# Performance work log

Measured on AMD Instinct MI355X. Metric: run time of the kernel, lower is better.

The kernel has to match this reference:

```python
import jax, jax.numpy as jnp
import numpy as np

EPS = 1e-5  # BatchNorm eps


def _conv_bn_tanh(h, w, b, g, be, m, v):
    # 3x3 conv, stride 1, SAME padding (pad = k//2), NCHW / OIHW
    y = jax.lax.conv_general_dilated(
        h, w, window_strides=(1, 1), padding='SAME',
        dimension_numbers=('NCHW', 'OIHW', 'NCHW'))
    y = y + b[None, :, None, None]
    # BatchNorm inference: gamma * (y - mean) / sqrt(var + eps) + beta
    scale = g * jax.lax.rsqrt(v + EPS)
    y = y * scale[None, :, None, None] + (be - m * scale)[None, :, None, None]
    return jnp.tanh(y)


def _unfold3x3(x):
    # torch F.unfold(k=3, pad=1, stride=1) -> (N, C, 9, H, W), kernel positions row-major
    N, C, H, W = x.shape
    xp = jnp.pad(x, ((0, 0), (0, 0), (1, 1), (1, 1)))
    patches = [xp[:, :, i:i + H, j:j + W] for i in range(3) for j in range(3)]
    return jnp.stack(patches, axis=2)  # (N, C, 9, H, W)


def setup_inputs() -> dict:
    key = jax.random.key(0)
    ks = jax.random.split(key, 24)
    N, C, H, W = 8, 64, 128, 128
    INTER, FEAT, NB, KK = 64, 6, 6, 9
    d = {}
    d['x'] = jax.random.normal(ks[0], (N, C, H, W), jnp.float32)
    d['w0'] = jax.random.normal(ks[1], (INTER, C, 3, 3), jnp.float32) * 0.05
    d['b0'] = jax.random.normal(ks[2], (INTER,), jnp.float32) * 0.05
    d['g0'] = jax.random.uniform(ks[3], (INTER,), jnp.float32)
    d['be0'] = jax.random.normal(ks[4], (INTER,), jnp.float32) * 0.05
    d['m0'] = jax.random.normal(ks[5], (INTER,), jnp.float32) * 0.05
    d['v0'] = jax.random.uniform(ks[6], (INTER,), jnp.float32)
    d['wm'] = jax.random.normal(ks[7], (5, INTER, INTER, 3, 3), jnp.float32) * 0.05
    d['bm'] = jax.random.normal(ks[8], (5, INTER), jnp.float32) * 0.05
    d['gm'] = jax.random.uniform(ks[9], (5, INTER), jnp.float32)
    d['bem'] = jax.random.normal(ks[10], (5, INTER), jnp.float32) * 0.05
    d['mm'] = jax.random.normal(ks[11], (5, INTER), jnp.float32) * 0.05
    d['vm'] = jax.random.uniform(ks[12], (5, INTER), jnp.float32)
    OC = FEAT * NB  # 36
    d['wl'] = jax.random.normal(ks[13], (OC, INTER, 3, 3), jnp.float32) * 0.05
    d['bl'] = jax.random.normal(ks[14], (OC,), jnp.float32) * 0.05
    d['gl'] = jax.random.uniform(ks[15], (OC,), jnp.float32)
    d['bel'] = jax.random.normal(ks[16], (OC,), jnp.float32) * 0.05
    d['ml'] = jax.random.normal(ks[17], (OC,), jnp.float32) * 0.05
    d['vl'] = jax.random.uniform(ks[18], (OC,), jnp.float32)
    d['bases'] = jax.random.normal(ks[19], (NB, KK), jnp.float32)  # FB bases buffer (6, 9)
    return d


def reference(x, w0, b0, g0, be0, m0, v0, wm, bm, gm, bem, mm, vm,
              wl, bl, gl, bel, ml, vl, bases):
    N, C, H, W = x.shape
    FEAT, NB = 6, 6
    # bases_net: conv-bn-tanh x7 (eval mode, dropout no-ops)
    h = _conv_bn_tanh(x, w0, b0, g0, be0, m0, v0)
    for i in range(5):
        h = _conv_bn_tanh(h, wm[i], bm[i], gm[i], bem[i], mm[i], vm[i])
    h = _conv_bn_tanh(h, wl, bl, gl, bel, ml, vl)  # (N, 36, H, W)
    bfeat = h.reshape(N, FEAT, NB, H, W)
    # per-pixel basis coefficients: (N, M, 9, H, W)
    bcoef = jnp.einsum('bmkhw,kl->bmlhw', bfeat, bases)
    patches = _unfold3x3(x)  # (N, C, 9, H, W)
    # dynamic conv: combine per-pixel coeffs with unfolded input
    out = jnp.einsum('bmlhw,bclhw->bcmhw', bcoef, patches)  # (N, C, M, H, W)
    return out.reshape(N, C * NB, H, W)
```

## Files before the change

kernel.cpp:

```cpp
#include <hip/hip_runtime.h>
#include <hip/hip_bf16.h>

typedef short bf16x4 __attribute__((ext_vector_type(4)));
typedef short bf16x8 __attribute__((ext_vector_type(8)));
typedef float f32x4  __attribute__((ext_vector_type(4)));

__device__ inline unsigned short f2us(float f) {
    __hip_bfloat16 h = __float2bfloat16(f);
    return *(unsigned short*)&h;
}
__device__ inline float us2f(unsigned short u) {
    union { unsigned int i; float f; } c; c.i = ((unsigned int)u) << 16; return c.f;
}
__device__ inline float tanh_fast(float x) {
    float xs = fminf(fmaxf(x, -20.f), 20.f);
    float t = __expf(2.f * xs);
    return 1.f - 2.f / (t + 1.f);
}

__device__ inline void gload_lds16(const void* g, void* l) {
    __builtin_amdgcn_global_load_lds(
        (const __attribute__((address_space(1))) void*)g,
        (__attribute__((address_space(3))) void*)l,
        16, 0, 0);
}

__global__ __launch_bounds__(256)
void prep_all(const float* __restrict__ x, unsigned short* __restrict__ xcl,
              const float* __restrict__ w0, const float* __restrict__ wm,
              const float* __restrict__ wl, unsigned short* __restrict__ Wf,
              const float* b0, const float* g0, const float* be0,
              const float* m0, const float* v0,
              const float* bm, const float* gm, const float* bem,
              const float* mm, const float* vm,
              const float* bl, const float* gl, const float* bel,
              const float* ml, const float* vl,
              float* __restrict__ Af, float* __restrict__ Bf,
              unsigned int* __restrict__ zp)
{
    const int bid = blockIdx.x;
    const int t = threadIdx.x;
    if (bid < 1024) {
        __shared__ unsigned short t2[128 * 68];
        int n = bid >> 7, h = bid & 127;
        const float* xp = x + (size_t)n * 64 * 16384 + h * 128;
        for (int i = t; i < 8192; i += 256) {
            int ci = i >> 7, w = i & 127;
            t2[w * 68 + ci] = f2us(xp[(size_t)ci * 16384 + w]);
        }
        __syncthreads();
        unsigned short* op = xcl + ((size_t)(n * 16384 + h * 128)) * 64;
        for (int i = t; i < 1024; i += 256) {
            int w = i >> 3, c8 = i & 7;
            union { bf16x4 v[2]; uint4 q; } u;
            u.v[0] = *(bf16x4*)&t2[w * 68 + c8 * 8];
            u.v[1] = *(bf16x4*)&t2[w * 68 + c8 * 8 + 4];
            *(uint4*)(op + w * 64 + c8 * 8) = u.q;
        }
    } else if (bid < 2032) {
        int idx = (bid - 1024) * 256 + t;
        int l = idx / 36864, r = idx - l * 36864;
        int tp = r >> 12, r2 = r & 4095;
        int hh = r2 >> 11, nb = (r2 >> 9) & 3, ln = (r2 >> 3) & 63, j = r2 & 7;
        int ci = hh * 32 + (ln >> 4) * 8 + j;
        int co = (ln & 15) * 4 + nb;
        float val = 0.f;
        if (l < 6) {
            const float* src = (l == 0) ? w0 : (wm + (size_t)(l - 1) * 36864);
            val = src[(co * 64 + ci) * 9 + tp];
        } else if (co < 36) {
            val = wl[(co * 64 + ci) * 9 + tp];
        }
        Wf[idx] = f2us(val);
    } else {
        int idx = (bid - 2032) * 256 + t;
        if (bid == 2033 && t >= 192) zp[t - 192] = 0u;
        if (idx < 448) {
            int l = idx >> 6, c = idx & 63;
            float b, g, be, m, v;
            bool zero = false;
            if (l == 0) {
                b = b0[c]; g = g0[c]; be = be0[c]; m = m0[c]; v = v0[c];
            } else if (l < 6) {
                int o = (l - 1) * 64 + c;
                b = bm[o]; g = gm[o]; be = bem[o]; m = mm[o]; v = vm[o];
            } else if (c < 36) {
                b = bl[c]; g = gl[c]; be = bel[c]; m = ml[c]; v = vl[c];
            } else zero = true;
            if (zero) { Af[idx] = 0.f; Bf[idx] = 0.f; }
            else {
                float s = g / sqrtf(v + 1e-5f);
                Af[idx] = s;
                Bf[idx] = (b - m) * s + be;
            }
        }
    }
}

#define LDS_W_OFF 78336
__global__ __launch_bounds__(512, 2)
void conv_mfma(const unsigned short* __restrict__ src,
               const unsigned short* __restrict__ Wf,
               const float* __restrict__ A, const float* __restrict__ B,
               unsigned short* __restrict__ dst,
               const unsigned short* __restrict__ zp)
{
    __shared__ __align__(16) unsigned char smem[152064];
    const int n = blockIdx.z;
    const int h0 = blockIdx.y * 16, w0 = blockIdx.x * 32;
    const int t = threadIdx.x;
    const int ln = t & 63, wv = t >> 6;
    const int xln = ln & 15, qd = ln >> 4;
    const size_t ibase = (size_t)n * 16384 * 64;

    const unsigned short* srcn = src + ibase;
    for (int i = wv; i < 77; i += 8) {
        int g = i * 64 + ln;
        int p = g >> 3, jj = g & 7;
        int ty = (p * 1928) >> 16;
        int tx = p - ty * 34;
        int gy = h0 + ty - 1, gx = w0 + tx - 1;
        int js = jj ^ (p & 7);
        const unsigned short* gsrc =
            (((unsigned)gy < 128u) & ((unsigned)gx < 128u))
                ? srcn + (ptrdiff_t)(gy * 128 + gx) * 64 + js * 8
                : zp;
        if (g < 4896) gload_lds16(gsrc, smem + (size_t)i * 1024);
    }
    for (int i = wv; i < 72; i += 8) {
        const unsigned short* gsrc = Wf + ((size_t)(i * 64 + ln)) * 8;
        gload_lds16(gsrc, smem + LDS_W_OFF + (size_t)i * 1024);
    }
    __syncthreads();

    f32x4 acc[2][2][4];
#pragma unroll
    for (int rh = 0; rh < 2; ++rh)
#pragma unroll
        for (int hf = 0; hf < 2; ++hf)
#pragma unroll
            for (int nb = 0; nb < 4; ++nb)
                acc[rh][hf][nb] = (f32x4){0.f, 0.f, 0.f, 0.f};

    const int rbase = wv * 2;
#pragma unroll
    for (int tp = 0; tp < 9; ++tp) {
        const int ky = tp / 3, kx = tp % 3;
        bf16x8 b[2][4];
#pragma unroll
        for (int hh = 0; hh < 2; ++hh)
#pragma unroll
            for (int nb = 0; nb < 4; ++nb)
                b[hh][nb] = *(const bf16x8*)(smem + LDS_W_OFF +
                    (((((tp * 2 + hh) * 4 + nb) * 64) + ln) << 4));
#pragma unroll
        for (int rh = 0; rh < 2; ++rh) {
#pragma unroll
            for (int hf = 0; hf < 2; ++hf) {
                const int p = (rbase + rh + ky) * 34 + hf * 16 + xln + kx;
                const int pb = p * 128, sw = (p & 7) << 4;
#pragma unroll
                for (int hh = 0; hh < 2; ++hh) {
                    bf16x8 a = *(const bf16x8*)(smem + pb +
                                                (((qd + 4 * hh) << 4) ^ sw));
#pragma unroll
                    for (int nb = 0; nb < 4; ++nb)
                        acc[rh][hf][nb] = __builtin_amdgcn_mfma_f32_16x16x32_bf16(
                            a, b[hh][nb], acc[rh][hf][nb], 0, 0, 0);
                }
            }
        }
    }

    const float4 A4 = *(const float4*)&A[xln * 4];
    const float4 B4 = *(const float4*)&B[xln * 4];
#pragma unroll
    for (int rh = 0; rh < 2; ++rh) {
        const int gy = h0 + rbase + rh;
        unsigned short* dp = dst + ibase + (size_t)(gy * 128) * 64 + xln * 4;
#pragma unroll
        for (int hf = 0; hf < 2; ++hf) {
#pragma unroll
            for (int r = 0; r < 4; ++r) {
                const int gx = w0 + hf * 16 + qd * 4 + r;
                ushort4 o;
                o.x = f2us(tanh_fast(fmaf(acc[rh][hf][0][r], A4.x, B4.x)));
                o.y = f2us(tanh_fast(fmaf(acc[rh][hf][1][r], A4.y, B4.y)));
                o.z = f2us(tanh_fast(fmaf(acc[rh][hf][2][r], A4.z, B4.z)));
                o.w = f2us(tanh_fast(fmaf(acc[rh][hf][3][r], A4.w, B4.w)));
                *(ushort4*)(dp + (size_t)gx * 64) = o;
            }
        }
    }
}

__global__ __launch_bounds__(256)
void dyn_conv(const float* __restrict__ x, const unsigned short* __restrict__ h7,
              const float* __restrict__ bases, float* __restrict__ out)
{
    __shared__ float tile[32 * 10 * 34];
    const int n = blockIdx.z;
    const int h0 = blockIdx.y * 8, w0 = blockIdx.x * 32;
    const float* xp = x + (size_t)n * 64 * 16384;
    const int t = threadIdx.x;
    const int tw = t & 31, th = t >> 5;
    const int h = h0 + th, w = w0 + tw;

    float bs[54];
#pragma unroll
    for (int i = 0; i < 54; ++i) bs[i] = bases[i];

    union { uint4 q[5]; unsigned short s[40]; } hv;
    const unsigned short* hp = h7 + (size_t)(n * 16384 + h * 128 + w) * 64;
#pragma unroll
    for (int i = 0; i < 5; ++i) hv.q[i] = ((const uint4*)hp)[i];

    float coef[54];
#pragma unroll
    for (int i = 0; i < 54; ++i) coef[i] = 0.f;
#pragma unroll
    for (int m = 0; m < 6; ++m)
#pragma unroll
        for (int k = 0; k < 6; ++k) {
            float f = us2f(hv.s[m * 6 + k]);
#pragma unroll
            for (int l = 0; l < 9; ++l)
                coef[m * 9 + l] = fmaf(f, bs[k * 9 + l], coef[m * 9 + l]);
        }

    float* op = out + (size_t)n * 384 * 16384 + h * 128 + w;

    for (int half = 0; half < 2; ++half) {
        if (half) __syncthreads();
        for (int idx = t; idx < 32 * 340; idx += 256) {
            int ci = idx / 340, r = idx % 340, y = r / 34, xw = r % 34;
            int gy = h0 + y - 1, gx = w0 + xw - 1;
            float v = 0.f;
            if ((unsigned)gy < 128u && (unsigned)gx < 128u)
                v = xp[(size_t)(half * 32 + ci) * 16384 + gy * 128 + gx];
            tile[idx] = v;
        }
        __syncthreads();

#pragma unroll 1
        for (int c = 0; c < 32; ++c) {
            float xv[9];
#pragma unroll
            for (int ky = 0; ky < 3; ++ky)
#pragma unroll
                for (int kx = 0; kx < 3; ++kx)
                    xv[ky * 3 + kx] = tile[c * 340 + (th + ky) * 34 + (tw + kx)];
            int cg = half * 32 + c;
#pragma unroll
            for (int m = 0; m < 6; ++m) {
                float s = 0.f;
#pragma unroll
                for (int l = 0; l < 9; ++l) s = fmaf(coef[m * 9 + l], xv[l], s);
                op[(size_t)(cg * 6 + m) * 16384] = s;
            }
        }
    }
}

extern "C" void kernel_launch(void* const* d_in, const int* in_sizes, int n_in,
                              void* d_out, int out_size, void* d_ws, size_t ws_size,
                              hipStream_t stream)
{
    const float* x   = (const float*)d_in[0];
    const float* w0  = (const float*)d_in[1];
    const float* b0  = (const float*)d_in[2];
    const float* g0  = (const float*)d_in[3];
    const float* be0 = (const float*)d_in[4];
    const float* m0  = (const float*)d_in[5];
    const float* v0  = (const float*)d_in[6];
    const float* wm  = (const float*)d_in[7];
    const float* bm  = (const float*)d_in[8];
    const float* gm  = (const float*)d_in[9];
    const float* bem = (const float*)d_in[10];
    const float* mm  = (const float*)d_in[11];
    const float* vm  = (const float*)d_in[12];
    const float* wl  = (const float*)d_in[13];
    const float* bl  = (const float*)d_in[14];
    const float* gl  = (const float*)d_in[15];
    const float* bel = (const float*)d_in[16];
    const float* ml  = (const float*)d_in[17];
    const float* vl  = (const float*)d_in[18];
    const float* bas = (const float*)d_in[19];

    unsigned short* Wfb = (unsigned short*)d_ws;
    float* Af  = (float*)((char*)d_ws + 524288);
    float* Bf  = Af + 448;
    unsigned int* zp = (unsigned int*)((char*)d_ws + (1 << 20));
    unsigned short* xcl  = (unsigned short*)((char*)d_ws + (size_t)(2  << 20));
    unsigned short* bufA = (unsigned short*)((char*)d_ws + (size_t)(2  << 20) + 16777216);
    unsigned short* bufB = (unsigned short*)((char*)d_ws + (size_t)(2  << 20) + 2 * 16777216);

    prep_all<<<2034, 256, 0, stream>>>(x, xcl, w0, wm, wl, Wfb,
                                       b0, g0, be0, m0, v0,
                                       bm, gm, bem, mm, vm,
                                       bl, gl, bel, ml, vl, Af, Bf, zp);

    dim3 cg(4, 8, 8);
    const unsigned short* zps = (const unsigned short*)zp;
    conv_mfma<<<cg, 512, 0, stream>>>(xcl,  Wfb + 0 * 36864, Af + 0,   Bf + 0,   bufA, zps);
    conv_mfma<<<cg, 512, 0, stream>>>(bufA, Wfb + 1 * 36864, Af + 64,  Bf + 64,  bufB, zps);
    conv_mfma<<<cg, 512, 0, stream>>>(bufB, Wfb + 2 * 36864, Af + 128, Bf + 128, bufA, zps);
    conv_mfma<<<cg, 512, 0, stream>>>(bufA, Wfb + 3 * 36864, Af + 192, Bf + 192, bufB, zps);
    conv_mfma<<<cg, 512, 0, stream>>>(bufB, Wfb + 4 * 36864, Af + 256, Bf + 256, bufA, zps);
    conv_mfma<<<cg, 512, 0, stream>>>(bufA, Wfb + 5 * 36864, Af + 320, Bf + 320, bufB, zps);
    conv_mfma<<<cg, 512, 0, stream>>>(bufB, Wfb + 6 * 36864, Af + 384, Bf + 384, bufA, zps);

    dim3 dg(4, 16, 8);
    dyn_conv<<<dg, 256, 0, stream>>>(x, bufA, bas, (float*)d_out);
}
```

Baseline: 403.7 us.

## Fuse all stages into one cooperative persistent kernel with grid syncs

Replaces the prep kernel, the seven conv launches and the dynamic-conv kernel with a single cooperative kernel of 256 persistent blocks that use grid.sync between stages. Each block keeps its tile resident in LDS across layers, reloads only its interior tile before the barrier and the halo after it, and prefetches the next layer's weights into registers during the epilogue. This is meant to remove launch gaps and redundant LDS reloads. In exchange it adds grid-wide barrier cost, limits the grid to 256 blocks so occupancy is fixed, and reworks the dyn_conv tiling to 512 threads.

```diff
diff --git a/kernel.cpp b/kernel.cpp
--- a/kernel.cpp
+++ b/kernel.cpp
@@ -1,5 +1,8 @@
 #include <hip/hip_runtime.h>
 #include <hip/hip_bf16.h>
+#include <hip/hip_cooperative_groups.h>
+
+namespace cg = cooperative_groups;
 
 typedef short bf16x4 __attribute__((ext_vector_type(4)));
 typedef short bf16x8 __attribute__((ext_vector_type(8)));
@@ -25,238 +28,298 @@
         16, 0, 0);
 }
 
-__global__ __launch_bounds__(256)
-void prep_all(const float* __restrict__ x, unsigned short* __restrict__ xcl,
-              const float* __restrict__ w0, const float* __restrict__ wm,
-              const float* __restrict__ wl, unsigned short* __restrict__ Wf,
-              const float* b0, const float* g0, const float* be0,
-              const float* m0, const float* v0,
-              const float* bm, const float* gm, const float* bem,
-              const float* mm, const float* vm,
-              const float* bl, const float* gl, const float* bel,
-              const float* ml, const float* vl,
-              float* __restrict__ Af, float* __restrict__ Bf,
-              unsigned int* __restrict__ zp)
+struct MegaArgs {
+    const float *x, *w0, *b0, *g0, *be0, *m0, *v0;
+    const float *wm, *bm, *gm, *bem, *mm, *vm;
+    const float *wl, *bl, *gl, *bel, *ml, *vl, *bas;
+    unsigned short *Wfb, *xcl, *bufA, *bufB;
+    float *Af, *Bf, *out;
+    unsigned int *zp;
+};
+
+#define LDS_W_OFF 78336
+
+__global__ __launch_bounds__(512, 2) void mega(MegaArgs g)
 {
+    __shared__ __align__(16) unsigned char smem[152064];
     const int bid = blockIdx.x;
     const int t = threadIdx.x;
-    if (bid < 1024) {
-        __shared__ unsigned short t2[128 * 68];
-        int n = bid >> 7, h = bid & 127;
-        const float* xp = x + (size_t)n * 64 * 16384 + h * 128;
-        for (int i = t; i < 8192; i += 256) {
-            int ci = i >> 7, w = i & 127;
-            t2[w * 68 + ci] = f2us(xp[(size_t)ci * 16384 + w]);
-        }
-        __syncthreads();
-        unsigned short* op = xcl + ((size_t)(n * 16384 + h * 128)) * 64;
-        for (int i = t; i < 1024; i += 256) {
-            int w = i >> 3, c8 = i & 7;
-            union { bf16x4 v[2]; uint4 q; } u;
-            u.v[0] = *(bf16x4*)&t2[w * 68 + c8 * 8];
-            u.v[1] = *(bf16x4*)&t2[w * 68 + c8 * 8 + 4];
-            *(uint4*)(op + w * 64 + c8 * 8) = u.q;
-        }
-    } else if (bid < 2032) {
-        int idx = (bid - 1024) * 256 + t;
-        int l = idx / 36864, r = idx - l * 36864;
-        int tp = r >> 12, r2 = r & 4095;
-        int hh = r2 >> 11, nb = (r2 >> 9) & 3, ln = (r2 >> 3) & 63, j = r2 & 7;
-        int ci = hh * 32 + (ln >> 4) * 8 + j;
-        int co = (ln & 15) * 4 + nb;
-        float val = 0.f;
-        if (l < 6) {
-            const float* src = (l == 0) ? w0 : (wm + (size_t)(l - 1) * 36864);
-            val = src[(co * 64 + ci) * 9 + tp];
-        } else if (co < 36) {
-            val = wl[(co * 64 + ci) * 9 + tp];
-        }
-        Wf[idx] = f2us(val);
-    } else {
-        int idx = (bid - 2032) * 256 + t;
-        if (bid == 2033 && t >= 192) zp[t - 192] = 0u;
-        if (idx < 448) {
-            int l = idx >> 6, c = idx & 63;
-            float b, g, be, m, v;
+    const int ln = t & 63, wv = t >> 6;
+    cg::grid_group grid = cg::this_grid();
+
+    {
+        unsigned short* t2 = (unsigned short*)smem;
+        for (int k = 0; k < 4; ++k) {
+            int tid = bid * 4 + k;
+            int pn = tid >> 7, ph = tid & 127;
+            const float* xp = g.x + (size_t)pn * 64 * 16384 + ph * 128;
+            if (k) __syncthreads();
+            for (int i = t; i < 8192; i += 512) {
+                int ci = i >> 7, w = i & 127;
+                t2[w * 68 + ci] = f2us(xp[(size_t)ci * 16384 + w]);
+            }
+            __syncthreads();
+            unsigned short* op = g.xcl + ((size_t)(pn * 16384 + ph * 128)) * 64;
+            for (int i = t; i < 1024; i += 512) {
+                int w = i >> 3, c8 = i & 7;
+                union { bf16x4 v[2]; uint4 q; } u;
+                u.v[0] = *(bf16x4*)&t2[w * 68 + c8 * 8];
+                u.v[1] = *(bf16x4*)&t2[w * 68 + c8 * 8 + 4];
+                *(uint4*)(op + w * 64 + c8 * 8) = u.q;
+            }
+        }
+        for (int j = t; j < 1008; j += 512) {
+            int idx = bid * 1008 + j;
+            int l = idx / 36864, r = idx - l * 36864;
+            int tp = r >> 12, r2 = r & 4095;
+            int hh = r2 >> 11, nb = (r2 >> 9) & 3, lw = (r2 >> 3) & 63, jc = r2 & 7;
+            int ci = hh * 32 + (lw >> 4) * 8 + jc;
+            int co = (lw & 15) * 4 + nb;
+            float val = 0.f;
+            if (l < 6) {
+                const float* s0 = (l == 0) ? g.w0 : (g.wm + (size_t)(l - 1) * 36864);
+                val = s0[(co * 64 + ci) * 9 + tp];
+            } else if (co < 36) {
+                val = g.wl[(co * 64 + ci) * 9 + tp];
+            }
+            g.Wfb[idx] = f2us(val);
+        }
+        if (bid == 0 && t < 448) {
+            int l = t >> 6, c = t & 63;
+            float b, ga, be, m, v;
             bool zero = false;
             if (l == 0) {
-                b = b0[c]; g = g0[c]; be = be0[c]; m = m0[c]; v = v0[c];
+                b = g.b0[c]; ga = g.g0[c]; be = g.be0[c]; m = g.m0[c]; v = g.v0[c];
             } else if (l < 6) {
                 int o = (l - 1) * 64 + c;
-                b = bm[o]; g = gm[o]; be = bem[o]; m = mm[o]; v = vm[o];
+                b = g.bm[o]; ga = g.gm[o]; be = g.bem[o]; m = g.mm[o]; v = g.vm[o];
             } else if (c < 36) {
-                b = bl[c]; g = gl[c]; be = bel[c]; m = ml[c]; v = vl[c];
+                b = g.bl[c]; ga = g.gl[c]; be = g.bel[c]; m = g.ml[c]; v = g.vl[c];
             } else zero = true;
-            if (zero) { Af[idx] = 0.f; Bf[idx] = 0.f; }
+            if (zero) { g.Af[t] = 0.f; g.Bf[t] = 0.f; }
             else {
-                float s = g / sqrtf(v + 1e-5f);
-                Af[idx] = s;
-                Bf[idx] = (b - m) * s + be;
-            }
-        }
+                float s = ga / sqrtf(v + 1e-5f);
+                g.Af[t] = s;
+                g.Bf[t] = (b - m) * s + be;
+            }
+        }
+        if (bid == 1 && t < 64) g.zp[t] = 0u;
     }
-}
-
-#define LDS_W_OFF 78336
-__global__ __launch_bounds__(512, 2)
-void conv_mfma(const unsigned short* __restrict__ src,
-               const unsigned short* __restrict__ Wf,
-               const float* __restrict__ A, const float* __restrict__ B,
-               unsigned short* __restrict__ dst,
-               const unsigned short* __restrict__ zp)
-{
-    __shared__ __align__(16) unsigned char smem[152064];
-    const int n = blockIdx.z;
-    const int h0 = blockIdx.y * 16, w0 = blockIdx.x * 32;
-    const int t = threadIdx.x;
-    const int ln = t & 63, wv = t >> 6;
+    grid.sync();
+
+    const int bx = bid & 3, by = (bid >> 2) & 7, cn = bid >> 5;
+    const int h0 = by * 16, w0c = bx * 32;
+    const size_t ibase = (size_t)cn * 16384 * 64;
     const int xln = ln & 15, qd = ln >> 4;
-    const size_t ibase = (size_t)n * 16384 * 64;
-
-    const unsigned short* srcn = src + ibase;
-    for (int i = wv; i < 77; i += 8) {
-        int g = i * 64 + ln;
-        int p = g >> 3, jj = g & 7;
-        int ty = (p * 1928) >> 16;
-        int tx = p - ty * 34;
-        int gy = h0 + ty - 1, gx = w0 + tx - 1;
-        int js = jj ^ (p & 7);
-        const unsigned short* gsrc =
-            (((unsigned)gy < 128u) & ((unsigned)gx < 128u))
-                ? srcn + (ptrdiff_t)(gy * 128 + gx) * 64 + js * 8
-                : zp;
-        if (g < 4896) gload_lds16(gsrc, smem + (size_t)i * 1024);
+    const int rbase = wv * 2;
+    uint4 wpre[9];
+
+    {
+        const unsigned short* srcn = g.xcl + ibase;
+        for (int i = wv; i < 77; i += 8) {
+            int gg = i * 64 + ln;
+            int p = gg >> 3, jj = gg & 7;
+            int ty = (p * 1928) >> 16;
+            int tx = p - ty * 34;
+            int gy = h0 + ty - 1, gx = w0c + tx - 1;
+            int js = jj ^ (p & 7);
+            const unsigned short* gsrc =
+                (((unsigned)gy < 128u) & ((unsigned)gx < 128u))
+                    ? srcn + (ptrdiff_t)(gy * 128 + gx) * 64 + js * 8
+                    : (const unsigned short*)g.zp;
+            if (gg < 4896) gload_lds16(gsrc, smem + (size_t)i * 1024);
+        }
+        for (int i = wv; i < 72; i += 8)
+            gload_lds16(g.Wfb + ((size_t)(i * 64 + ln)) * 8,
+                        smem + LDS_W_OFF + (size_t)i * 1024);
+        __syncthreads();
     }
-    for (int i = wv; i < 72; i += 8) {
-        const unsigned short* gsrc = Wf + ((size_t)(i * 64 + ln)) * 8;
-        gload_lds16(gsrc, smem + LDS_W_OFF + (size_t)i * 1024);
+
+#pragma unroll 1
+    for (int l = 0; l < 7; ++l) {
+        unsigned short* dstp = (l & 1) ? g.bufB : g.bufA;
+
+        f32x4 acc[2][2][4];
+#pragma unroll
+        for (int rh = 0; rh < 2; ++rh)
+#pragma unroll
+            for (int hf = 0; hf < 2; ++hf)
+#pragma unroll
+                for (int nb = 0; nb < 4; ++nb)
+                    acc[rh][hf][nb] = (f32x4){0.f, 0.f, 0.f, 0.f};
+
+#pragma unroll
+        for (int tp = 0; tp < 9; ++tp) {
+            const int ky = tp / 3, kx = tp % 3;
+            bf16x8 b[2][4];
+#pragma unroll
+            for (int hh = 0; hh < 2; ++hh)
+#pragma unroll
+                for (int nb = 0; nb < 4; ++nb)
+                    b[hh][nb] = *(const bf16x8*)(smem + LDS_W_OFF +
+                        (((((tp * 2 + hh) * 4 + nb) * 64) + ln) << 4));
+#pragma unroll
+            for (int rh = 0; rh < 2; ++rh) {
+#pragma unroll
+                for (int hf = 0; hf < 2; ++hf) {
+                    const int p = (rbase + rh + ky) * 34 + hf * 16 + xln + kx;
+                    const int pb = p * 128, sw = (p & 7) << 4;
+#pragma unroll
+                    for (int hh = 0; hh < 2; ++hh) {
+                        bf16x8 a = *(const bf16x8*)(smem + pb +
+                                                    (((qd + 4 * hh) << 4) ^ sw));
+#pragma unroll
+                        for (int nb = 0; nb < 4; ++nb)
+                            acc[rh][hf][nb] = __builtin_amdgcn_mfma_f32_16x16x32_bf16(
+                                a, b[hh][nb], acc[rh][hf][nb], 0, 0, 0);
+                    }
+                }
+            }
+        }
+
+        if (l < 6) {
+            const uint4* wnext = (const uint4*)(g.Wfb + (size_t)(l + 1) * 36864);
+#pragma unroll
+            for (int k = 0; k < 9; ++k) wpre[k] = wnext[t + 512 * k];
+        }
+
+        {
+            const float* Ap = g.Af + l * 64;
+            const float* Bp = g.Bf + l * 64;
+            const float4 A4 = *(const float4*)&Ap[xln * 4];
+            const float4 B4 = *(const float4*)&Bp[xln * 4];
+#pragma unroll
+            for (int rh = 0; rh < 2; ++rh) {
+                const int gy = h0 + rbase + rh;
+                unsigned short* dp = dstp + ibase + (size_t)(gy * 128) * 64 + xln * 4;
+#pragma unroll
+                for (int hf = 0; hf < 2; ++hf) {
+#pragma unroll
+                    for (int r = 0; r < 4; ++r) {
+                        const int gx = w0c + hf * 16 + qd * 4 + r;
+                        ushort4 o;
+                        o.x = f2us(tanh_fast(fmaf(acc[rh][hf][0][r], A4.x, B4.x)));
+                        o.y = f2us(tanh_fast(fmaf(acc[rh][hf][1][r], A4.y, B4.y)));
+                        o.z = f2us(tanh_fast(fmaf(acc[rh][hf][2][r], A4.z, B4.z)));
+                        o.w = f2us(tanh_fast(fmaf(acc[rh][hf][3][r], A4.w, B4.w)));
+                        *(ushort4*)(dp + (size_t)gx * 64) = o;
+                    }
+                }
+            }
+        }
+        if (l == 6) break;
+
+        __threadfence();
+        __syncthreads();
+
+        const unsigned short* srcn = dstp + ibase;
+        for (int i = wv; i < 64; i += 8) {
+            int p = i * 8 + (ln >> 3), jj = ln & 7;
+            int ty = 1 + (p >> 5), tx = 1 + (p & 31);
+            int pp = ty * 34 + tx;
+            int gy = h0 + ty - 1, gx = w0c + tx - 1;
+            int js = jj ^ (pp & 7);
+            gload_lds16(srcn + (ptrdiff_t)(gy * 128 + gx) * 64 + js * 8,
+                        smem + (size_t)((1 + (i >> 2)) * 34 + 1 + (i & 3) * 8) * 128);
+        }
+
+        grid.sync();
+
+        for (int i = wv; i < 10; i += 8) {
+            int row = (i < 5) ? 0 : 17;
+            int i5 = (i < 5) ? i : i - 5;
+            int pir = i5 * 8 + (ln >> 3), jj = ln & 7;
+            int pp = row * 34 + pir;
+            int gy = h0 + row - 1, gx = w0c + pir - 1;
+            int js = jj ^ (pp & 7);
+            const unsigned short* gsrc =
+                (((unsigned)gy < 128u) & ((unsigned)gx < 128u))
+                    ? srcn + (ptrdiff_t)(gy * 128 + gx) * 64 + js * 8
+                    : (const unsigned short*)g.zp;
+            if (pir < 34) gload_lds16(gsrc, smem + (size_t)(row * 34 + i5 * 8) * 128);
+        }
+        if (t < 256) {
+            int k2 = t >> 3, jj = t & 7;
+            int ty = 1 + (k2 >> 1), tx = (k2 & 1) * 33;
+            int pp = ty * 34 + tx;
+            int gy = h0 + ty - 1, gx = w0c + tx - 1;
+            uint4 v = make_uint4(0u, 0u, 0u, 0u);
+            if ((unsigned)gx < 128u)
+                v = *(const uint4*)(srcn + (ptrdiff_t)(gy * 128 + gx) * 64 + jj * 8);
+            *(uint4*)(smem + (size_t)pp * 128 + ((size_t)(jj ^ (pp & 7)) << 4)) = v;
+        }
+        {
+            uint4* wdst = (uint4*)(smem + LDS_W_OFF);
+#pragma unroll
+            for (int k = 0; k < 9; ++k) wdst[t + 512 * k] = wpre[k];
+        }
+        __syncthreads();
     }
-    __syncthreads();
-
-    f32x4 acc[2][2][4];
-#pragma unroll
-    for (int rh = 0; rh < 2; ++rh)
-#pragma unroll
-        for (int hf = 0; hf < 2; ++hf)
-#pragma unroll
-            for (int nb = 0; nb < 4; ++nb)
-                acc[rh][hf][nb] = (f32x4){0.f, 0.f, 0.f, 0.f};
-
-    const int rbase = wv * 2;
-#pragma unroll
-    for (int tp = 0; tp < 9; ++tp) {
-        const int ky = tp / 3, kx = tp % 3;
-        bf16x8 b[2][4];
-#pragma unroll
-        for (int hh = 0; hh < 2; ++hh)
-#pragma unroll
-            for (int nb = 0; nb < 4; ++nb)
-                b[hh][nb] = *(const bf16x8*)(smem + LDS_W_OFF +
-                    (((((tp * 2 + hh) * 4 + nb) * 64) + ln) << 4));
-#pragma unroll
-        for (int rh = 0; rh < 2; ++rh) {
-#pragma unroll
-            for (int hf = 0; hf < 2; ++hf) {
-                const int p = (rbase + rh + ky) * 34 + hf * 16 + xln + kx;
-                const int pb = p * 128, sw = (p & 7) << 4;
-#pragma unroll
-                for (int hh = 0; hh < 2; ++hh) {
-                    bf16x8 a = *(const bf16x8*)(smem + pb +
-                                                (((qd + 4 * hh) << 4) ^ sw));
-#pragma unroll
-                    for (int nb = 0; nb < 4; ++nb)
-                        acc[rh][hf][nb] = __builtin_amdgcn_mfma_f32_16x16x32_bf16(
-                            a, b[hh][nb], acc[rh][hf][nb], 0, 0, 0);
+
+    grid.sync();
+
+    {
+        float* tile = (float*)smem;
+        const int dn = bid >> 5, ti = bid & 31;
+        const int h0d = (ti >> 1) * 8, w0d = (ti & 1) * 64;
+        const float* xp = g.x + (size_t)dn * 64 * 16384;
+        const int tw = t & 63, th = t >> 6;
+        const int h = h0d + th, w = w0d + tw;
+
+        float bs[54];
+#pragma unroll
+        for (int i = 0; i < 54; ++i) bs[i] = g.bas[i];
+
+        union { uint4 q[5]; unsigned short s[40]; } hv;
+        const unsigned short* hp = g.bufA + (size_t)(dn * 16384 + h * 128 + w) * 64;
+#pragma unroll
+        for (int i = 0; i < 5; ++i) hv.q[i] = ((const uint4*)hp)[i];
+
+        float coef[54];
+#pragma unroll
+        for (int i = 0; i < 54; ++i) coef[i] = 0.f;
+#pragma unroll
+        for (int m = 0; m < 6; ++m)
+#pragma unroll
+            for (int k = 0; k < 6; ++k) {
+                float f = us2f(hv.s[m * 6 + k]);
+#pragma unroll
+                for (int lq = 0; lq < 9; ++lq)
+                    coef[m * 9 + lq] = fmaf(f, bs[k * 9 + lq], coef[m * 9 + lq]);
+            }
+
+        float* op = g.out + (size_t)dn * 384 * 16384 + h * 128 + w;
+
+        for (int half = 0; half < 2; ++half) {
+            if (half) __syncthreads();
+            for (int idx = t; idx < 21120; idx += 512) {
+                int ci = idx / 660, r = idx - ci * 660;
+                int y = r / 66, xw = r - y * 66;
+                int gy = h0d + y - 1, gx = w0d + xw - 1;
+                float v = 0.f;
+                if ((unsigned)gy < 128u && (unsigned)gx < 128u)
+                    v = xp[(size_t)(half * 32 + ci) * 16384 + gy * 128 + gx];
+                tile[idx] = v;
+            }
+            __syncthreads();
+
+#pragma unroll 1
+            for (int c = 0; c < 32; ++c) {
+                float xv[9];
+#pragma unroll
+                for (int ky = 0; ky < 3; ++ky)
+#pragma unroll
+                    for (int kx = 0; kx < 3; ++kx)
+                        xv[ky * 3 + kx] = tile[c * 660 + (th + ky) * 66 + (tw + kx)];
+                int cgc = half * 32 + c;
+#pragma unroll
+                for (int m = 0; m < 6; ++m) {
+                    float s = 0.f;
+#pragma unroll
+                    for (int lq = 0; lq < 9; ++lq)
+                        s = fmaf(coef[m * 9 + lq], xv[lq], s);
+                    op[(size_t)(cgc * 6 + m) * 16384] = s;
                 }
-            }
-        }
-    }
-
-    const float4 A4 = *(const float4*)&A[xln * 4];
-    const float4 B4 = *(const float4*)&B[xln * 4];
-#pragma unroll
-    for (int rh = 0; rh < 2; ++rh) {
-        const int gy = h0 + rbase + rh;
-        unsigned short* dp = dst + ibase + (size_t)(gy * 128) * 64 + xln * 4;
-#pragma unroll
-        for (int hf = 0; hf < 2; ++hf) {
-#pragma unroll
-            for (int r = 0; r < 4; ++r) {
-                const int gx = w0 + hf * 16 + qd * 4 + r;
-                ushort4 o;
-                o.x = f2us(tanh_fast(fmaf(acc[rh][hf][0][r], A4.x, B4.x)));
-                o.y = f2us(tanh_fast(fmaf(acc[rh][hf][1][r], A4.y, B4.y)));
-                o.z = f2us(tanh_fast(fmaf(acc[rh][hf][2][r], A4.z, B4.z)));
-                o.w = f2us(tanh_fast(fmaf(acc[rh][hf][3][r], A4.w, B4.w)));
-                *(ushort4*)(dp + (size_t)gx * 64) = o;
-            }
-        }
-    }
-}
-
-__global__ __launch_bounds__(256)
-void dyn_conv(const float* __restrict__ x, const unsigned short* __restrict__ h7,
-              const float* __restrict__ bases, float* __restrict__ out)
-{
-    __shared__ float tile[32 * 10 * 34];
-    const int n = blockIdx.z;
-    const int h0 = blockIdx.y * 8, w0 = blockIdx.x * 32;
-    const float* xp = x + (size_t)n * 64 * 16384;
-    const int t = threadIdx.x;
-    const int tw = t & 31, th = t >> 5;
-    const int h = h0 + th, w = w0 + tw;
-
-    float bs[54];
-#pragma unroll
-    for (int i = 0; i < 54; ++i) bs[i] = bases[i];
-
-    union { uint4 q[5]; unsigned short s[40]; } hv;
-    const unsigned short* hp = h7 + (size_t)(n * 16384 + h * 128 + w) * 64;
-#pragma unroll
-    for (int i = 0; i < 5; ++i) hv.q[i] = ((const uint4*)hp)[i];
-
-    float coef[54];
-#pragma unroll
-    for (int i = 0; i < 54; ++i) coef[i] = 0.f;
-#pragma unroll
-    for (int m = 0; m < 6; ++m)
-#pragma unroll
-        for (int k = 0; k < 6; ++k) {
-            float f = us2f(hv.s[m * 6 + k]);
-#pragma unroll
-            for (int l = 0; l < 9; ++l)
-                coef[m * 9 + l] = fmaf(f, bs[k * 9 + l], coef[m * 9 + l]);
-        }
-
-    float* op = out + (size_t)n * 384 * 16384 + h * 128 + w;
-
-    for (int half = 0; half < 2; ++half) {
-        if (half) __syncthreads();
-        for (int idx = t; idx < 32 * 340; idx += 256) {
-            int ci = idx / 340, r = idx % 340, y = r / 34, xw = r % 34;
-            int gy = h0 + y - 1, gx = w0 + xw - 1;
-            float v = 0.f;
-            if ((unsigned)gy < 128u && (unsigned)gx < 128u)
-                v = xp[(size_t)(half * 32 + ci) * 16384 + gy * 128 + gx];
-            tile[idx] = v;
-        }
-        __syncthreads();
-
-#pragma unroll 1
-        for (int c = 0; c < 32; ++c) {
-            float xv[9];
-#pragma unroll
-            for (int ky = 0; ky < 3; ++ky)
-#pragma unroll
-                for (int kx = 0; kx < 3; ++kx)
-                    xv[ky * 3 + kx] = tile[c * 340 + (th + ky) * 34 + (tw + kx)];
-            int cg = half * 32 + c;
-#pragma unroll
-            for (int m = 0; m < 6; ++m) {
-                float s = 0.f;
-#pragma unroll
-                for (int l = 0; l < 9; ++l) s = fmaf(coef[m * 9 + l], xv[l], s);
-                op[(size_t)(cg * 6 + m) * 16384] = s;
             }
         }
     }
@@ -266,50 +329,37 @@
                               void* d_out, int out_size, void* d_ws, size_t ws_size,
                               hipStream_t stream)
 {
-    const float* x   = (const float*)d_in[0];
-    const float* w0  = (const float*)d_in[1];
-    const float* b0  = (const float*)d_in[2];
-    const float* g0  = (const float*)d_in[3];
-    const float* be0 = (const float*)d_in[4];
-    const float* m0  = (const float*)d_in[5];
-    const float* v0  = (const float*)d_in[6];
-    const float* wm  = (const float*)d_in[7];
-    const float* bm  = (const float*)d_in[8];
-    const float* gm  = (const float*)d_in[9];
-    const float* bem = (const float*)d_in[10];
-    const float* mm  = (const float*)d_in[11];
-    const float* vm  = (const float*)d_in[12];
-    const float* wl  = (const float*)d_in[13];
-    const float* bl  = (const float*)d_in[14];
-    const float* gl  = (const float*)d_in[15];
-    const float* bel = (const float*)d_in[16];
-    const float* ml  = (const float*)d_in[17];
-    const float* vl  = (const float*)d_in[18];
-    const float* bas = (const float*)d_in[19];
-
-    unsigned short* Wfb = (unsigned short*)d_ws;
-    float* Af  = (float*)((char*)d_ws + 524288);
-    float* Bf  = Af + 448;
-    unsigned int* zp = (unsigned int*)((char*)d_ws + (1 << 20));
-    unsigned short* xcl  = (unsigned short*)((char*)d_ws + (size_t)(2  << 20));
-    unsigned short* bufA = (unsigned short*)((char*)d_ws + (size_t)(2  << 20) + 16777216);
-    unsigned short* bufB = (unsigned short*)((char*)d_ws + (size_t)(2  << 20) + 2 * 16777216);
-
-    prep_all<<<2034, 256, 0, stream>>>(x, xcl, w0, wm, wl, Wfb,
-                                       b0, g0, be0, m0, v0,
-                                       bm, gm, bem, mm, vm,
-                                       bl, gl, bel, ml, vl, Af, Bf, zp);
-
-    dim3 cg(4, 8, 8);
-    const unsigned short* zps = (const unsigned short*)zp;
-    conv_mfma<<<cg, 512, 0, stream>>>(xcl,  Wfb + 0 * 36864, Af + 0,   Bf + 0,   bufA, zps);
-    conv_mfma<<<cg, 512, 0, stream>>>(bufA, Wfb + 1 * 36864, Af + 64,  Bf + 64,  bufB, zps);
-    conv_mfma<<<cg, 512, 0, stream>>>(bufB, Wfb + 2 * 36864, Af + 128, Bf + 128, bufA, zps);
-    conv_mfma<<<cg, 512, 0, stream>>>(bufA, Wfb + 3 * 36864, Af + 192, Bf + 192, bufB, zps);
-    conv_mfma<<<cg, 512, 0, stream>>>(bufB, Wfb + 4 * 36864, Af + 256, Bf + 256, bufA, zps);
-    conv_mfma<<<cg, 512, 0, stream>>>(bufA, Wfb + 5 * 36864, Af + 320, Bf + 320, bufB, zps);
-    conv_mfma<<<cg, 512, 0, stream>>>(bufB, Wfb + 6 * 36864, Af + 384, Bf + 384, bufA, zps);
-
-    dim3 dg(4, 16, 8);
-    dyn_conv<<<dg, 256, 0, stream>>>(x, bufA, bas, (float*)d_out);
-}
+    MegaArgs a;
+    a.x   = (const float*)d_in[0];
+    a.w0  = (const float*)d_in[1];
+    a.b0  = (const float*)d_in[2];
+    a.g0  = (const float*)d_in[3];
+    a.be0 = (const float*)d_in[4];
+    a.m0  = (const float*)d_in[5];
+    a.v0  = (const float*)d_in[6];
+    a.wm  = (const float*)d_in[7];
+    a.bm  = (const float*)d_in[8];
+    a.gm  = (const float*)d_in[9];
+    a.bem = (const float*)d_in[10];
+    a.mm  = (const float*)d_in[11];
+    a.vm  = (const float*)d_in[12];
+    a.wl  = (const float*)d_in[13];
+    a.bl  = (const float*)d_in[14];
+    a.gl  = (const float*)d_in[15];
+    a.bel = (const float*)d_in[16];
+    a.ml  = (const float*)d_in[17];
+    a.vl  = (const float*)d_in[18];
+    a.bas = (const float*)d_in[19];
+
+    a.Wfb  = (unsigned short*)d_ws;
+    a.Af   = (float*)((char*)d_ws + 524288);
+    a.Bf   = a.Af + 448;
+    a.zp   = (unsigned int*)((char*)d_ws + (1 << 20));
+    a.xcl  = (unsigned short*)((char*)d_ws + (size_t)(2 << 20));
+    a.bufA = (unsigned short*)((char*)d_ws + (size_t)(2 << 20) + 16777216);
+    a.bufB = (unsigned short*)((char*)d_ws + (size_t)(2 << 20) + 2 * 16777216);
+    a.out  = (float*)d_out;
+
+    void* ka[] = {&a};
+    hipLaunchCooperativeKernel((const void*)mega, dim3(256), dim3(512), ka, 0, stream);
+}
```

Result: slower. 979.7 us (+142.7%).

## Fuse last conv layer with dynamic convolution, keeping features in LDS

Applied to the files above, without the earlier changes.

Merges the seventh conv-bn-tanh layer into the dynamic-conv kernel. The per-pixel basis features are written to shared memory in a swizzled layout instead of a global buffer, then read back for the coefficient and patch combination. This removes one kernel launch and a global write/read of the intermediate feature map. In exchange, the dynamic-conv stage now runs with the conv kernel's tile shape and 16-row blocks, reusing the same large LDS buffer, which may lower occupancy.

```diff
diff --git a/kernel.cpp b/kernel.cpp
--- a/kernel.cpp
+++ b/kernel.cpp
@@ -194,26 +194,122 @@
     }
 }
 
-__global__ __launch_bounds__(256)
-void dyn_conv(const float* __restrict__ x, const unsigned short* __restrict__ h7,
-              const float* __restrict__ bases, float* __restrict__ out)
+__global__ __launch_bounds__(512, 2)
+void conv6_dyn(const unsigned short* __restrict__ src,
+               const unsigned short* __restrict__ Wf,
+               const float* __restrict__ A, const float* __restrict__ B,
+               const float* __restrict__ x, const float* __restrict__ bases,
+               float* __restrict__ out,
+               const unsigned short* __restrict__ zp)
 {
-    __shared__ float tile[32 * 10 * 34];
+    __shared__ __align__(16) unsigned char smem[152064];
     const int n = blockIdx.z;
-    const int h0 = blockIdx.y * 8, w0 = blockIdx.x * 32;
-    const float* xp = x + (size_t)n * 64 * 16384;
+    const int h0 = blockIdx.y * 16, w0 = blockIdx.x * 32;
     const int t = threadIdx.x;
-    const int tw = t & 31, th = t >> 5;
-    const int h = h0 + th, w = w0 + tw;
+    const int ln = t & 63, wv = t >> 6;
+    const int xln = ln & 15, qd = ln >> 4;
+    const size_t ibase = (size_t)n * 16384 * 64;
+
+    const unsigned short* srcn = src + ibase;
+    for (int i = wv; i < 77; i += 8) {
+        int g = i * 64 + ln;
+        int p = g >> 3, jj = g & 7;
+        int ty = (p * 1928) >> 16;
+        int tx = p - ty * 34;
+        int gy = h0 + ty - 1, gx = w0 + tx - 1;
+        int js = jj ^ (p & 7);
+        const unsigned short* gsrc =
+            (((unsigned)gy < 128u) & ((unsigned)gx < 128u))
+                ? srcn + (ptrdiff_t)(gy * 128 + gx) * 64 + js * 8
+                : zp;
+        if (g < 4896) gload_lds16(gsrc, smem + (size_t)i * 1024);
+    }
+    for (int i = wv; i < 72; i += 8) {
+        const unsigned short* gsrc = Wf + ((size_t)(i * 64 + ln)) * 8;
+        gload_lds16(gsrc, smem + LDS_W_OFF + (size_t)i * 1024);
+    }
+    __syncthreads();
+
+    f32x4 acc[2][2][4];
+#pragma unroll
+    for (int rh = 0; rh < 2; ++rh)
+#pragma unroll
+        for (int hf = 0; hf < 2; ++hf)
+#pragma unroll
+            for (int nb = 0; nb < 4; ++nb)
+                acc[rh][hf][nb] = (f32x4){0.f, 0.f, 0.f, 0.f};
+
+    const int rbase = wv * 2;
+#pragma unroll
+    for (int tp = 0; tp < 9; ++tp) {
+        const int ky = tp / 3, kx = tp % 3;
+        bf16x8 b[2][4];
+#pragma unroll
+        for (int hh = 0; hh < 2; ++hh)
+#pragma unroll
+            for (int nb = 0; nb < 4; ++nb)
+                b[hh][nb] = *(const bf16x8*)(smem + LDS_W_OFF +
+                    (((((tp * 2 + hh) * 4 + nb) * 64) + ln) << 4));
+#pragma unroll
+        for (int rh = 0; rh < 2; ++rh) {
+#pragma unroll
+            for (int hf = 0; hf < 2; ++hf) {
+                const int p = (rbase + rh + ky) * 34 + hf * 16 + xln + kx;
+                const int pb = p * 128, sw = (p & 7) << 4;
+#pragma unroll
+                for (int hh = 0; hh < 2; ++hh) {
+                    bf16x8 a = *(const bf16x8*)(smem + pb +
+                                                (((qd + 4 * hh) << 4) ^ sw));
+#pragma unroll
+                    for (int nb = 0; nb < 4; ++nb)
+                        acc[rh][hf][nb] = __builtin_amdgcn_mfma_f32_16x16x32_bf16(
+                            a, b[hh][nb], acc[rh][hf][nb], 0, 0, 0);
+                }
+            }
+        }
+    }
+    __syncthreads();
+
+    {
+        unsigned short* h7 = (unsigned short*)(smem + LDS_W_OFF);
+        const float4 A4 = *(const float4*)&A[xln * 4];
+        const float4 B4 = *(const float4*)&B[xln * 4];
+        const int cchunk = xln >> 1, coff = (xln & 1) * 8;
+#pragma unroll
+        for (int rh = 0; rh < 2; ++rh) {
+#pragma unroll
+            for (int hf = 0; hf < 2; ++hf) {
+#pragma unroll
+                for (int r = 0; r < 4; ++r) {
+                    const int pl = (rbase + rh) * 32 + hf * 16 + qd * 4 + r;
+                    ushort4 o;
+                    o.x = f2us(tanh_fast(fmaf(acc[rh][hf][0][r], A4.x, B4.x)));
+                    o.y = f2us(tanh_fast(fmaf(acc[rh][hf][1][r], A4.y, B4.y)));
+                    o.z = f2us(tanh_fast(fmaf(acc[rh][hf][2][r], A4.z, B4.z)));
+                    o.w = f2us(tanh_fast(fmaf(acc[rh][hf][3][r], A4.w, B4.w)));
+                    *(ushort4*)((unsigned char*)h7 + pl * 128 +
+                                (((cchunk ^ (pl & 7)) << 4) | coff)) = o;
+                }
+            }
+        }
+    }
+    __syncthreads();
+
+    const int pxx = t & 31, py = t >> 5;
+    const int h = h0 + py, w = w0 + pxx;
 
     float bs[54];
 #pragma unroll
     for (int i = 0; i < 54; ++i) bs[i] = bases[i];
 
     union { uint4 q[5]; unsigned short s[40]; } hv;
-    const unsigned short* hp = h7 + (size_t)(n * 16384 + h * 128 + w) * 64;
-#pragma unroll
-    for (int i = 0; i < 5; ++i) hv.q[i] = ((const uint4*)hp)[i];
+    {
+        const int pl = py * 32 + pxx;
+        const unsigned char* hb = smem + LDS_W_OFF + pl * 128;
+#pragma unroll
+        for (int j = 0; j < 5; ++j)
+            hv.q[j] = *(const uint4*)(hb + ((j ^ (pl & 7)) << 4));
+    }
 
     float coef[54];
 #pragma unroll
@@ -224,21 +320,26 @@
         for (int k = 0; k < 6; ++k) {
             float f = us2f(hv.s[m * 6 + k]);
 #pragma unroll
-            for (int l = 0; l < 9; ++l)
-                coef[m * 9 + l] = fmaf(f, bs[k * 9 + l], coef[m * 9 + l]);
-        }
-
+            for (int lq = 0; lq < 9; ++lq)
+                coef[m * 9 + lq] = fmaf(f, bs[k * 9 + lq], coef[m * 9 + lq]);
+        }
+
+    const float* xp = x + (size_t)n * 64 * 16384;
     float* op = out + (size_t)n * 384 * 16384 + h * 128 + w;
+    float* tile = (float*)smem;
 
     for (int half = 0; half < 2; ++half) {
         if (half) __syncthreads();
-        for (int idx = t; idx < 32 * 340; idx += 256) {
-            int ci = idx / 340, r = idx % 340, y = r / 34, xw = r % 34;
+        for (int idx = t; idx < 19584; idx += 512) {
+            int y = ((idx >> 6) * 3856) >> 16;
+            int rem = idx - y * 1088;
+            int ci = (rem * 1928) >> 16;
+            int xw = rem - ci * 34;
             int gy = h0 + y - 1, gx = w0 + xw - 1;
             float v = 0.f;
             if ((unsigned)gy < 128u && (unsigned)gx < 128u)
                 v = xp[(size_t)(half * 32 + ci) * 16384 + gy * 128 + gx];
-            tile[idx] = v;
+            tile[ci * 612 + y * 34 + xw] = v;
         }
         __syncthreads();
 
@@ -249,14 +350,15 @@
             for (int ky = 0; ky < 3; ++ky)
 #pragma unroll
                 for (int kx = 0; kx < 3; ++kx)
-                    xv[ky * 3 + kx] = tile[c * 340 + (th + ky) * 34 + (tw + kx)];
-            int cg = half * 32 + c;
+                    xv[ky * 3 + kx] = tile[c * 612 + (py + ky) * 34 + (pxx + kx)];
+            int cgc = half * 32 + c;
 #pragma unroll
             for (int m = 0; m < 6; ++m) {
                 float s = 0.f;
 #pragma unroll
-                for (int l = 0; l < 9; ++l) s = fmaf(coef[m * 9 + l], xv[l], s);
-                op[(size_t)(cg * 6 + m) * 16384] = s;
+                for (int lq = 0; lq < 9; ++lq)
+                    s = fmaf(coef[m * 9 + lq], xv[lq], s);
+                op[(size_t)(cgc * 6 + m) * 16384] = s;
             }
         }
     }
@@ -308,8 +410,6 @@
     conv_mfma<<<cg, 512, 0, stream>>>(bufA, Wfb + 3 * 36864, Af + 192, Bf + 192, bufB, zps);
     conv_mfma<<<cg, 512, 0, stream>>>(bufB, Wfb + 4 * 36864, Af + 256, Bf + 256, bufA, zps);
     conv_mfma<<<cg, 512, 0, stream>>>(bufA, Wfb + 5 * 36864, Af + 320, Bf + 320, bufB, zps);
-    conv_mfma<<<cg, 512, 0, stream>>>(bufB, Wfb + 6 * 36864, Af + 384, Bf + 384, bufA, zps);
-
-    dim3 dg(4, 16, 8);
-    dyn_conv<<<dg, 256, 0, stream>>>(x, bufA, bas, (float*)d_out);
-}
+    conv6_dyn<<<cg, 512, 0, stream>>>(bufB, Wfb + 6 * 36864, Af + 384, Bf + 384,
+                                      x, bas, (float*)d_out, zps);
+}
```

Result: no change. 404.0 us (+0.1%).
